# Performance work log

Measured on AMD Instinct MI355X. Metric: run time of the kernel, lower is better.

The kernel has to match this reference:

```python
import jax, jax.numpy as jnp
import numpy as np

C = 256   # channel
NH = 8    # n_heads
NP = 8    # n_points (n_levels = 1)
HD = C // NH


def conv1x1(x, W, b):
    # x: [B,C,H,W], W: [Cout,Cin] -> 1x1 conv == channel-mixing GEMM
    return jnp.einsum('bchw,oc->bohw', x, W) + b[None, :, None, None]


def linear(x, W, b):
    # x: [B,Q,Cin], W: [Cout,Cin] (torch nn.Linear layout)
    return jnp.einsum('bqc,oc->bqo', x, W) + b


def msda(value, loc, attn_w, H, Wd):
    # Multi-scale deformable attention core (single level).
    # value:  [B,Q,NH,HD]  (Q = H*Wd)
    # loc:    [B,Q,NH,NP,2] normalized sampling locations in [0,1] (x,y)
    # attn_w: [B,Q,NH,NP]  softmax weights
    B, Q = value.shape[0], value.shape[1]
    v = jnp.transpose(value, (0, 2, 1, 3))  # [B,NH,HW,HD]
    # grid_sample(align_corners=False): pixel coord = loc*size - 0.5
    ix = loc[..., 0] * Wd - 0.5
    iy = loc[..., 1] * H - 0.5
    x0 = jnp.floor(ix)
    y0 = jnp.floor(iy)

    def gather(xi, yi, wgt):
        valid = ((xi >= 0) & (xi < Wd) & (yi >= 0) & (yi < H)).astype(wgt.dtype)
        xc = jnp.clip(xi, 0, Wd - 1).astype(jnp.int32)
        yc = jnp.clip(yi, 0, H - 1).astype(jnp.int32)
        idx = yc * Wd + xc                                  # [B,Q,NH,NP]
        idx = jnp.transpose(idx, (0, 2, 1, 3)).reshape(B, NH, Q * NP)
        s = jnp.take_along_axis(v, idx[..., None], axis=2)  # [B,NH,Q*NP,HD]
        s = s.reshape(B, NH, Q, NP, HD)
        w = jnp.transpose(wgt * valid, (0, 2, 1, 3))[..., None]
        return s * w

    acc = (gather(x0, y0, (x0 + 1 - ix) * (y0 + 1 - iy))
           + gather(x0 + 1, y0, (ix - x0) * (y0 + 1 - iy))
           + gather(x0, y0 + 1, (x0 + 1 - ix) * (iy - y0))
           + gather(x0 + 1, y0 + 1, (ix - x0) * (iy - y0)))
    aw = jnp.transpose(attn_w, (0, 2, 1, 3))[..., None]      # [B,NH,Q,NP,1]
    out = (acc * aw).sum(axis=3)                             # [B,NH,Q,HD]
    return jnp.transpose(out, (0, 2, 1, 3)).reshape(B, Q, C)


def setup_inputs() -> dict:
    key = jax.random.key(0)
    ks = jax.random.split(key, 24)
    B, H, W = 2, 128, 128

    def w(k, shape, s=0.02):
        return jax.random.normal(k, shape, jnp.float32) * s

    d = {
        'xt': jax.random.normal(ks[0], (B, C, H, W), jnp.float32),
        'xt_1': jax.random.normal(ks[1], (B, C, H, W), jnp.float32),
        'W_in1': w(ks[2], (C, C)), 'b_in1': jnp.zeros((C,), jnp.float32),
        'W_in2': w(ks[3], (C, C)), 'b_in2': jnp.zeros((C,), jnp.float32),
        'Wv': w(ks[4], (C, C)), 'bv': jnp.zeros((C,), jnp.float32),
        'Ws': w(ks[5], (NH * NP * 2, C)), 'bs_off': w(ks[6], (NH * NP * 2,), 1.0),
        'Wa': w(ks[7], (NH * NP, C)), 'ba': jnp.zeros((NH * NP,), jnp.float32),
        'Wo': w(ks[8], (C, C)), 'bo': jnp.zeros((C,), jnp.float32),
        'Wt1': w(ks[9], (C, C)), 'bt1': jnp.zeros((C,), jnp.float32),
        'Wt2': w(ks[10], (C, C)), 'bt2': jnp.zeros((C,), jnp.float32),
        'Wout': w(ks[11], (C, C)), 'bout': jnp.zeros((C,), jnp.float32),
    }
    return d


def reference(xt, xt_1, W_in1, b_in1, W_in2, b_in2, Wv, bv, Ws, bs_off,
              Wa, ba, Wo, bo, Wt1, bt1, Wt2, bt2, Wout, bout):
    x1 = conv1x1(xt, W_in1, b_in1)
    x2 = conv1x1(xt_1, W_in2, b_in2)
    B, _, H, Wd = x1.shape
    Q = H * Wd
    q = jnp.transpose(x1, (0, 2, 3, 1)).reshape(B, Q, C)       # queries
    vflat = jnp.transpose(x2, (0, 2, 3, 1)).reshape(B, Q, C)   # values

    value = linear(vflat, Wv, bv).reshape(B, Q, NH, HD)
    offsets = linear(q, Ws, bs_off).reshape(B, Q, NH, NP, 2)
    attn = jax.nn.softmax(linear(q, Wa, ba).reshape(B, Q, NH, NP), axis=-1)

    # reference points at pixel centers, normalized (x,y)
    gy, gx = jnp.meshgrid(jnp.arange(H), jnp.arange(Wd), indexing='ij')
    ref = jnp.stack([(gx.reshape(-1) + 0.5) / Wd,
                     (gy.reshape(-1) + 0.5) / H], axis=-1).astype(jnp.float32)
    norm = jnp.array([Wd, H], jnp.float32)
    loc = ref[None, :, None, None, :] + offsets / norm          # [B,Q,NH,NP,2]

    out = msda(value, loc, attn, H, Wd)                         # [B,Q,C]
    xt_star = jnp.transpose(linear(out, Wo, bo), (0, 2, 1)).reshape(B, C, H, Wd)

    tg = conv1x1(jax.nn.relu(conv1x1(x1 * xt_star, Wt1, bt1)), Wt2, bt2)
    return jax.nn.relu(conv1x1(x1 + tg, Wout, bout))
```

## Files before the change

kernel.cpp:

```cpp
#include <hip/hip_runtime.h>
#include <math.h>


#define PIX 16384
#define BATCH 2
#define CH 256

typedef short bf16x8 __attribute__((ext_vector_type(8)));
typedef float f32x4 __attribute__((ext_vector_type(4)));

typedef const __attribute__((address_space(1))) void* as1cv;
typedef __attribute__((address_space(3))) void* as3v;
__device__ __forceinline__ void gl_lds16(const void* g, void* l) {
  __builtin_amdgcn_global_load_lds((as1cv)g, (as3v)l, 16, 0, 0);
}

__device__ __forceinline__ ushort f2bf(float f) {
  union { float f; unsigned u; } v; v.f = f;
  unsigned u = v.u;
  unsigned r = u + 0x7fffu + ((u >> 16) & 1u);
  return (ushort)(r >> 16);
}
__device__ __forceinline__ float bfl(unsigned u) {
  union { unsigned u; float f; } v; v.u = u << 16; return v.f;
}
__device__ __forceinline__ float bfh(unsigned u) {
  union { unsigned u; float f; } v; v.u = u & 0xffff0000u; return v.f;
}
__device__ __forceinline__ unsigned fuse_u32(unsigned a, unsigned b, bool mul) {
  float rl = mul ? bfl(a) * bfl(b) : bfl(a) + bfl(b);
  float rh = mul ? bfh(a) * bfh(b) : bfh(a) + bfh(b);
  return (unsigned)f2bf(rl) | ((unsigned)f2bf(rh) << 16);
}

__global__ __launch_bounds__(256) void prep_k(
    const float* __restrict__ xt, const float* __restrict__ xt_1,
    ushort* __restrict__ s0, ushort* __restrict__ s1,
    const float* __restrict__ W_in1, const float* __restrict__ Wo,
    const float* __restrict__ Wt1, const float* __restrict__ Wt2,
    const float* __restrict__ Wout, const float* __restrict__ Ws,
    const float* __restrict__ Wa, const float* __restrict__ bs_off,
    const float* __restrict__ ba, ushort* __restrict__ wb,
    float* __restrict__ bsa,
    const float* __restrict__ Wv, const float* __restrict__ W_in2,
    const float* __restrict__ b_in2, const float* __restrict__ bv,
    ushort* __restrict__ wvp, float* __restrict__ bvp)
{
  __shared__ float lds[32][33];
  const int bid = blockIdx.x;
  const int tid = threadIdx.x;

  if (bid < 16384) {
    const int z = bid >> 12;
    const int rem = bid & 4095;
    const int pblk = rem & 511, cblk = rem >> 9;
    const int b = z & 1;
    const float* in = (z < 2) ? xt : xt_1;
    ushort* out = (z < 2) ? s0 : s1;
    const int p0 = pblk * 32, c0 = cblk * 32;
    const int tx = tid & 31, ty = tid >> 5;
    const float* inb = in + (size_t)b * CH * PIX;
    #pragma unroll
    for (int i = 0; i < 4; ++i)
      lds[ty + i * 8][tx] = inb[(size_t)(c0 + ty + i * 8) * PIX + p0 + tx];
    __syncthreads();
    const int cx = (tid & 15) * 2, py = tid >> 4;
    ushort* outb = out + (size_t)b * PIX * CH;
    #pragma unroll
    for (int i = 0; i < 2; ++i) {
      int pl = py + i * 16;
      unsigned lo = f2bf(lds[cx][pl]);
      unsigned hi = f2bf(lds[cx + 1][pl]);
      *(unsigned*)(outb + (size_t)(p0 + pl) * CH + c0 + cx) = lo | (hi << 16);
    }
  } else if (bid < 16384 + 1473) {
    const int blk = bid - 16384;
    const int k = tid;
    if (blk >= 1472) {
      if (k < 128) bsa[k] = bs_off[k];
      else if (k < 192) bsa[k] = ba[k - 128];
      return;
    }
    const float* src;
    if (blk < 256) src = W_in1 + (size_t)blk * 256;
    else if (blk < 512) src = Wo + (size_t)(blk - 256) * 256;
    else if (blk < 768) src = Wt1 + (size_t)(blk - 512) * 256;
    else if (blk < 1024) src = Wt2 + (size_t)(blk - 768) * 256;
    else if (blk < 1280) src = Wout + (size_t)(blk - 1024) * 256;
    else if (blk < 1408) src = Ws + (size_t)(blk - 1280) * 256;
    else src = Wa + (size_t)(blk - 1408) * 256;
    wb[(size_t)blk * 256 + k] = f2bf(src[k]);
  } else {
    const int o = bid - (16384 + 1473 + 256 - 256) - 1473 - 16384 + 0;
    const int oo = bid - 17857;
    const int k = tid;
    float acc = 0.f;
    #pragma unroll 8
    for (int c = 0; c < 256; ++c)
      acc += Wv[(size_t)oo * 256 + c] * W_in2[(size_t)c * 256 + k];
    wvp[(size_t)oo * 256 + k] = f2bf(acc);
    float* red = &lds[0][0];
    red[k] = Wv[(size_t)oo * 256 + k] * b_in2[k];
    __syncthreads();
    for (int s = 128; s > 0; s >>= 1) {
      if (k < s) red[k] += red[k + s];
      __syncthreads();
    }
    if (k == 0) bvp[oo] = red[0] + bv[oo];
    (void)o;
  }
}

template<int FUSE, bool RELU, int OMODE>
__global__ __launch_bounds__(256, 4) void gemm2_k(
    const ushort* __restrict__ in, const ushort* __restrict__ in2,
    const ushort* __restrict__ Wb, const float* __restrict__ bias,
    void* __restrict__ out, int ldo, size_t obstride)
{
  constexpr int SMEMSZ = (OMODE == 0) ? 24576 : 34816;
  __shared__ __align__(16) char smem[SMEMSZ];
  const int tid = threadIdx.x;
  const int b = blockIdx.z;
  const int p0 = blockIdx.x * 128;
  const int o0 = blockIdx.y * 64;

  const ushort* inb = in + (size_t)b * PIX * CH;

  const int srow = tid >> 2;
  const int sseg = tid & 3;
  const int swz0 = (srow >> 1) & 3;
  const int swz1 = ((srow + 64) >> 1) & 3;
  const int gseg0 = (FUSE == 0) ? (sseg ^ swz0) : sseg;
  const int gseg1 = (FUSE == 0) ? (sseg ^ swz1) : sseg;
  const ushort* xsrc0 = inb + (size_t)(p0 + srow) * CH + gseg0 * 8;
  const ushort* xsrc1 = inb + (size_t)(p0 + srow + 64) * CH + gseg1 * 8;
  const ushort* x2src0 = (FUSE != 0)
      ? in2 + (size_t)b * PIX * CH + (size_t)(p0 + srow) * CH + sseg * 8 : (const ushort*)nullptr;
  const ushort* x2src1 = (FUSE != 0)
      ? in2 + (size_t)b * PIX * CH + (size_t)(p0 + srow + 64) * CH + sseg * 8 : (const ushort*)nullptr;
  const ushort* wsrc = Wb + (size_t)(o0 + srow) * CH + gseg0 * 8;

  const int l = tid & 63, wv = tid >> 6;
  const int lr = l & 15, g4 = l >> 4;

  f32x4 acc[2][4];
  #pragma unroll
  for (int i = 0; i < 2; ++i)
    #pragma unroll
    for (int j = 0; j < 4; ++j) acc[i][j] = (f32x4){0.f, 0.f, 0.f, 0.f};

  uint4 xr[2], x2r[2], wr;

#define STAGE_GLL(buf, kb)                                                     \
  {                                                                            \
    gl_lds16(xsrc0 + (kb), smem + (buf) * 8192 + tid * 16);                    \
    gl_lds16(xsrc1 + (kb), smem + (buf) * 8192 + 4096 + tid * 16);             \
    gl_lds16(wsrc + (kb), smem + 16384 + (buf) * 4096 + tid * 16);             \
  }

#define LOADT(kb)                                                              \
  {                                                                            \
    xr[0] = *(const uint4*)(xsrc0 + (kb));                                     \
    xr[1] = *(const uint4*)(xsrc1 + (kb));                                     \
    x2r[0] = *(const uint4*)(x2src0 + (kb));                                   \
    x2r[1] = *(const uint4*)(x2src1 + (kb));                                   \
    wr = *(const uint4*)(wsrc + (kb));                                         \
  }

#define WRITET(buf)                                                            \
  {                                                                            \
    _Pragma("unroll")                                                          \
    for (int r = 0; r < 2; ++r) {                                              \
      uint4 v = xr[r];                                                         \
      unsigned* pa = (unsigned*)&v;                                            \
      const unsigned* pb = (const unsigned*)&x2r[r];                           \
      _Pragma("unroll")                                                        \
      for (int w = 0; w < 4; ++w) pa[w] = fuse_u32(pa[w], pb[w], FUSE == 1);   \
      const int sw = r ? swz1 : swz0;                                          \
      *(uint4*)(smem + (buf) * 8192 + r * 4096 + srow * 64 +                   \
                ((sseg ^ sw) * 16)) = v;                                       \
    }                                                                          \
    *(uint4*)(smem + 16384 + (buf) * 4096 + srow * 64 +                        \
              ((sseg ^ swz0) * 16)) = wr;                                      \
  }

  if (FUSE == 0) { STAGE_GLL(0, 0) }
  else           { LOADT(0) WRITET(0) }
  __syncthreads();

  for (int t = 0; t < 8; ++t) {
    if (t < 7) {
      if (FUSE == 0) { STAGE_GLL((t + 1) & 1, (t + 1) * 32) }
      else           { LOADT((t + 1) * 32) }
    }
    const char* XB = smem + (t & 1) * 8192;
    const char* WB = smem + 16384 + (t & 1) * 4096;
    bf16x8 af[2], bfr[4];
    #pragma unroll
    for (int fm = 0; fm < 2; ++fm) {
      const int p = wv * 32 + fm * 16 + lr;
      af[fm] = *(const bf16x8*)(XB + p * 64 + ((g4 ^ ((p >> 1) & 3)) * 16));
    }
    #pragma unroll
    for (int fn = 0; fn < 4; ++fn) {
      const int o = fn * 16 + lr;
      bfr[fn] = *(const bf16x8*)(WB + o * 64 + ((g4 ^ ((o >> 1) & 3)) * 16));
    }
    #pragma unroll
    for (int fm = 0; fm < 2; ++fm)
      #pragma unroll
      for (int fn = 0; fn < 4; ++fn)
        acc[fm][fn] = __builtin_amdgcn_mfma_f32_16x16x32_bf16(af[fm], bfr[fn], acc[fm][fn], 0, 0, 0);
    if (t < 7 && FUSE != 0) { WRITET((t + 1) & 1) }
    __syncthreads();
  }
#undef STAGE_GLL
#undef LOADT
#undef WRITET

  float bvv[4];
  #pragma unroll
  for (int fn = 0; fn < 4; ++fn) bvv[fn] = bias[o0 + fn * 16 + lr];

  if (OMODE == 1) {
    float* El2 = (float*)smem;
    #pragma unroll
    for (int fm = 0; fm < 2; ++fm)
      #pragma unroll
      for (int fn = 0; fn < 4; ++fn) {
        float4 v;
        v.x = acc[fm][fn][0] + bvv[fn]; v.y = acc[fm][fn][1] + bvv[fn];
        v.z = acc[fm][fn][2] + bvv[fn]; v.w = acc[fm][fn][3] + bvv[fn];
        if (RELU) {
          v.x = fmaxf(v.x, 0.f); v.y = fmaxf(v.y, 0.f);
          v.z = fmaxf(v.z, 0.f); v.w = fmaxf(v.w, 0.f);
        }
        *(float4*)&El2[(size_t)(fn * 16 + lr) * 132 + wv * 32 + fm * 16 + g4 * 4] = v;
      }
    __syncthreads();
    float* outb = (float*)out + (size_t)b * obstride;
    const int og = tid >> 5, seg = tid & 31;
    #pragma unroll
    for (int r = 0; r < 8; ++r) {
      const int orow = og + r * 8;
      float4 v = *(float4*)(smem + orow * 528 + seg * 16);
      *(float4*)(outb + (size_t)(o0 + orow) * ldo + p0 + seg * 4) = v;
    }
  } else {
    ushort* El = (ushort*)smem;
    #pragma unroll
    for (int fm = 0; fm < 2; ++fm)
      #pragma unroll
      for (int fn = 0; fn < 4; ++fn)
        #pragma unroll
        for (int r = 0; r < 4; ++r) {
          const int p = wv * 32 + fm * 16 + g4 * 4 + r;
          float v = acc[fm][fn][r] + bvv[fn];
          if (RELU) v = fmaxf(v, 0.f);
          El[p * 72 + fn * 16 + lr] = f2bf(v);
        }
    __syncthreads();
    ushort* outb = (ushort*)out + (size_t)b * obstride;
    const int rg = tid >> 3, seg = tid & 7;
    #pragma unroll
    for (int r = 0; r < 4; ++r) {
      const int row = rg + r * 32;
      uint4 v = *(uint4*)(smem + row * 144 + seg * 16);
      *(uint4*)(outb + (size_t)(p0 + row) * ldo + o0 + seg * 8) = v;
    }
  }
}

__global__ __launch_bounds__(256, 4) void gemm2_dual_k(
    const ushort* __restrict__ inA, const ushort* __restrict__ inB,
    const ushort* __restrict__ WbA, const ushort* __restrict__ WbB,
    const float* __restrict__ biasA, const float* __restrict__ biasB,
    ushort* __restrict__ outA, ushort* __restrict__ outB)
{
  __shared__ __align__(16) char smem[24576];
  const int tid = threadIdx.x;
  const int b = blockIdx.z;
  const int p0 = blockIdx.x * 128;
  const bool second = blockIdx.y >= 4;
  const int o0 = (blockIdx.y & 3) * 64;
  const ushort* in = second ? inB : inA;
  const ushort* Wb = second ? WbB : WbA;
  const float* bias = second ? biasB : biasA;
  ushort* out = second ? outB : outA;

  const ushort* inb = in + (size_t)b * PIX * CH;

  const int srow = tid >> 2;
  const int sseg = tid & 3;
  const int swz0 = (srow >> 1) & 3;
  const int swz1 = ((srow + 64) >> 1) & 3;
  const int gseg0 = sseg ^ swz0;
  const int gseg1 = sseg ^ swz1;
  const ushort* xsrc0 = inb + (size_t)(p0 + srow) * CH + gseg0 * 8;
  const ushort* xsrc1 = inb + (size_t)(p0 + srow + 64) * CH + gseg1 * 8;
  const ushort* wsrc = Wb + (size_t)(o0 + srow) * CH + gseg0 * 8;

  const int l = tid & 63, wv = tid >> 6;
  const int lr = l & 15, g4 = l >> 4;

  f32x4 acc[2][4];
  #pragma unroll
  for (int i = 0; i < 2; ++i)
    #pragma unroll
    for (int j = 0; j < 4; ++j) acc[i][j] = (f32x4){0.f, 0.f, 0.f, 0.f};

#define STAGE_GLL(buf, kb)                                                     \
  {                                                                            \
    gl_lds16(xsrc0 + (kb), smem + (buf) * 8192 + tid * 16);                    \
    gl_lds16(xsrc1 + (kb), smem + (buf) * 8192 + 4096 + tid * 16);             \
    gl_lds16(wsrc + (kb), smem + 16384 + (buf) * 4096 + tid * 16);             \
  }

  STAGE_GLL(0, 0)
  __syncthreads();

  for (int t = 0; t < 8; ++t) {
    if (t < 7) { STAGE_GLL((t + 1) & 1, (t + 1) * 32) }
    const char* XB = smem + (t & 1) * 8192;
    const char* WB = smem + 16384 + (t & 1) * 4096;
    bf16x8 af[2], bfr[4];
    #pragma unroll
    for (int fm = 0; fm < 2; ++fm) {
      const int p = wv * 32 + fm * 16 + lr;
      af[fm] = *(const bf16x8*)(XB + p * 64 + ((g4 ^ ((p >> 1) & 3)) * 16));
    }
    #pragma unroll
    for (int fn = 0; fn < 4; ++fn) {
      const int o = fn * 16 + lr;
      bfr[fn] = *(const bf16x8*)(WB + o * 64 + ((g4 ^ ((o >> 1) & 3)) * 16));
    }
    #pragma unroll
    for (int fm = 0; fm < 2; ++fm)
      #pragma unroll
      for (int fn = 0; fn < 4; ++fn)
        acc[fm][fn] = __builtin_amdgcn_mfma_f32_16x16x32_bf16(af[fm], bfr[fn], acc[fm][fn], 0, 0, 0);
    __syncthreads();
  }
#undef STAGE_GLL

  float bvv[4];
  #pragma unroll
  for (int fn = 0; fn < 4; ++fn) bvv[fn] = bias[o0 + fn * 16 + lr];

  ushort* El = (ushort*)smem;
  #pragma unroll
  for (int fm = 0; fm < 2; ++fm)
    #pragma unroll
    for (int fn = 0; fn < 4; ++fn)
      #pragma unroll
      for (int r = 0; r < 4; ++r) {
        const int p = wv * 32 + fm * 16 + g4 * 4 + r;
        El[p * 72 + fn * 16 + lr] = f2bf(acc[fm][fn][r] + bvv[fn]);
      }
  __syncthreads();
  ushort* outb = out + (size_t)b * PIX * CH;
  const int rg = tid >> 3, seg = tid & 7;
  #pragma unroll
  for (int r = 0; r < 4; ++r) {
    const int row = rg + r * 32;
    uint4 v = *(uint4*)(smem + row * 144 + seg * 16);
    *(uint4*)(outb + (size_t)(p0 + row) * CH + o0 + seg * 8) = v;
  }
}

__global__ __launch_bounds__(256) void msda_k(
    const ushort* __restrict__ value, const ushort* __restrict__ sa,
    ushort* __restrict__ out)
{
  const int t = blockIdx.x * 256 + threadIdx.x;
  const int dh = t & 1;
  const int h = (t >> 1) & 7;
  const int pg = t >> 4;
  const int b = pg >> 14;
  const int p = pg & (PIX - 1);
  const int px = p & 127, py = p >> 7;

  const ushort* vb = value + (size_t)b * PIX * CH;
  const ushort* sp = sa + (size_t)pg * 192;

  uint4 lgv = *(const uint4*)(sp + 128 + h * 8);
  const unsigned* lgw = (const unsigned*)&lgv;
  float lg[8];
  #pragma unroll
  for (int i = 0; i < 4; ++i) { lg[2 * i] = bfl(lgw[i]); lg[2 * i + 1] = bfh(lgw[i]); }
  float m = lg[0];
  #pragma unroll
  for (int i = 1; i < 8; ++i) m = fmaxf(m, lg[i]);
  float s = 0.f;
  #pragma unroll
  for (int i = 0; i < 8; ++i) { lg[i] = __expf(lg[i] - m); s += lg[i]; }
  const float inv = 1.f / s;

  uint4 ov0 = *(const uint4*)(sp + h * 16);
  uint4 ov1 = *(const uint4*)(sp + h * 16 + 8);
  float of[16];
  {
    const unsigned* ow = (const unsigned*)&ov0;
    #pragma unroll
    for (int i = 0; i < 4; ++i) { of[2 * i] = bfl(ow[i]); of[2 * i + 1] = bfh(ow[i]); }
    const unsigned* ow1 = (const unsigned*)&ov1;
    #pragma unroll
    for (int i = 0; i < 4; ++i) { of[8 + 2 * i] = bfl(ow1[i]); of[8 + 2 * i + 1] = bfh(ow1[i]); }
  }

  float acc[16];
  #pragma unroll
  for (int i = 0; i < 16; ++i) acc[i] = 0.f;

  #pragma unroll
  for (int pt = 0; pt < 8; ++pt) {
    const float ox = of[2 * pt], oy = of[2 * pt + 1];
    const float aw = lg[pt] * inv;
    const float ix = px + ox, iy = py + oy;
    const float xf = floorf(ix), yf = floorf(iy);
    const float fx = ix - xf, fy = iy - yf;
    const int x0 = (int)xf, y0 = (int)yf;
    #pragma unroll
    for (int cr = 0; cr < 4; ++cr) {
      const int dx = cr & 1, dy = cr >> 1;
      const int xx = x0 + dx, yy = y0 + dy;
      const float wx = dx ? fx : (1.f - fx);
      const float wy = dy ? fy : (1.f - fy);
      const bool valid = ((unsigned)xx < 128u) & ((unsigned)yy < 128u);
      float w = valid ? (wx * wy * aw) : 0.f;
      const int xc = min(max(xx, 0), 127), yc = min(max(yy, 0), 127);
      const ushort* vr = vb + ((size_t)(yc * 128 + xc) * CH + h * 32 + dh * 16);
      uint4 q0 = *(const uint4*)vr;
      uint4 q1 = *(const uint4*)(vr + 8);
      const unsigned* qw0 = (const unsigned*)&q0;
      const unsigned* qw1 = (const unsigned*)&q1;
      #pragma unroll
      for (int ww = 0; ww < 4; ++ww) {
        acc[2 * ww + 0] = fmaf(w, bfl(qw0[ww]), acc[2 * ww + 0]);
        acc[2 * ww + 1] = fmaf(w, bfh(qw0[ww]), acc[2 * ww + 1]);
        acc[8 + 2 * ww + 0] = fmaf(w, bfl(qw1[ww]), acc[8 + 2 * ww + 0]);
        acc[8 + 2 * ww + 1] = fmaf(w, bfh(qw1[ww]), acc[8 + 2 * ww + 1]);
      }
    }
  }
  unsigned r[8];
  #pragma unroll
  for (int k = 0; k < 8; ++k)
    r[k] = (unsigned)f2bf(acc[2 * k]) | ((unsigned)f2bf(acc[2 * k + 1]) << 16);
  ushort* dst = out + (size_t)pg * CH + h * 32 + dh * 16;
  *(uint4*)dst = *(uint4*)&r[0];
  *(uint4*)(dst + 8) = *(uint4*)&r[4];
}

extern "C" void kernel_launch(void* const* d_in, const int* in_sizes, int n_in,
                              void* d_out, int out_size, void* d_ws, size_t ws_size,
                              hipStream_t stream)
{
  const float* xt     = (const float*)d_in[0];
  const float* xt_1   = (const float*)d_in[1];
  const float* W_in1  = (const float*)d_in[2];
  const float* b_in1  = (const float*)d_in[3];
  const float* W_in2  = (const float*)d_in[4];
  const float* b_in2  = (const float*)d_in[5];
  const float* Wv     = (const float*)d_in[6];
  const float* bv     = (const float*)d_in[7];
  const float* Ws     = (const float*)d_in[8];
  const float* bs_off = (const float*)d_in[9];
  const float* Wa     = (const float*)d_in[10];
  const float* ba     = (const float*)d_in[11];
  const float* Wo     = (const float*)d_in[12];
  const float* bo     = (const float*)d_in[13];
  const float* Wt1    = (const float*)d_in[14];
  const float* bt1    = (const float*)d_in[15];
  const float* Wt2    = (const float*)d_in[16];
  const float* bt2    = (const float*)d_in[17];
  const float* Wout   = (const float*)d_in[18];
  const float* bout   = (const float*)d_in[19];

  char* ws = (char*)d_ws;
  const size_t SLOT = (size_t)BATCH * PIX * CH * 2;
  const size_t SAB  = (size_t)BATCH * PIX * 192 * 2;
  ushort* s0 = (ushort*)(ws + 0 * SLOT);
  ushort* s1 = (ushort*)(ws + 1 * SLOT);
  ushort* s2 = (ushort*)(ws + 2 * SLOT);
  ushort* s3 = (ushort*)(ws + 3 * SLOT);
  ushort* s4 = (ushort*)(ws + 4 * SLOT);
  ushort* sa = (ushort*)(ws + 5 * SLOT);
  char* wbase = ws + 5 * SLOT + SAB;
  ushort* wb  = (ushort*)wbase;
  ushort* wvp = (ushort*)(wbase + (size_t)1472 * 256 * 2);
  float* bsa  = (float*)(wbase + (size_t)1472 * 256 * 2 + (size_t)256 * 256 * 2);
  float* bvp  = bsa + 192;

  ushort* wb_in1 = wb;
  ushort* wb_o   = wb + 65536;
  ushort* wb_t1  = wb + 131072;
  ushort* wb_t2  = wb + 196608;
  ushort* wb_out = wb + 262144;
  ushort* wb_sa  = wb + 327680;

  dim3 blk(256);
  dim3 gD(PIX / 128, 8, BATCH);
  dim3 gF(PIX / 128, 4, BATCH);
  dim3 gS(PIX / 128, 3, BATCH);
  const size_t OBS = (size_t)PIX * CH;

  prep_k<<<18113, blk, 0, stream>>>(xt, xt_1, s0, s1,
      W_in1, Wo, Wt1, Wt2, Wout, Ws, Wa, bs_off, ba, wb, bsa,
      Wv, W_in2, b_in2, bv, wvp, bvp);

  gemm2_dual_k<<<gD, blk, 0, stream>>>(s0, s1, wb_in1, wvp, b_in1, bvp, s2, s3);
  gemm2_k<0, false, 0><<<gS, blk, 0, stream>>>(s2, nullptr, wb_sa, bsa, sa, 192, (size_t)PIX * 192);
  msda_k<<<dim3((BATCH * PIX * 16) / 256), blk, 0, stream>>>(s3, sa, s4);
  gemm2_k<0, false, 0><<<gF, blk, 0, stream>>>(s4, nullptr, wb_o, bo, s0, CH, OBS);
  gemm2_k<1, true , 0><<<gF, blk, 0, stream>>>(s0, s2, wb_t1, bt1, s1, CH, OBS);
  gemm2_k<0, false, 0><<<gF, blk, 0, stream>>>(s1, nullptr, wb_t2, bt2, s3, CH, OBS);
  gemm2_k<2, true , 1><<<gF, blk, 0, stream>>>(s3, s2, wb_out, bout, d_out, PIX, (size_t)CH * PIX);
}
```

Measured before the change: 155.2 us.

## Fuse back-to-back GEMM pairs into one kernel keeping intermediates in LDS

Replaces four separate 1x1-conv GEMM launches (Wo, Wt1, Wt2, Wout) with two fused kernels. Each kernel loads a 32-pixel tile of input and x1 into LDS, computes the first GEMM, writes its bf16 result back into LDS, then applies the elementwise fuse with x1 and the second GEMM. This removes two full intermediate round trips to global memory and two launches. In exchange each block uses 64KB of LDS, which lowers occupancy, and the tiles are smaller with weights re-streamed per block. The gemm2_k paths for FUSE and OMODE 1 are deleted as no longer used.

```diff
diff --git a/kernel.cpp b/kernel.cpp
--- a/kernel.cpp
+++ b/kernel.cpp
@@ -91,7 +91,6 @@
     else src = Wa + (size_t)(blk - 1408) * 256;
     wb[(size_t)blk * 256 + k] = f2bf(src[k]);
   } else {
-    const int o = bid - (16384 + 1473 + 256 - 256) - 1473 - 16384 + 0;
     const int oo = bid - 17857;
     const int k = tid;
     float acc = 0.f;
@@ -107,7 +106,6 @@
       __syncthreads();
     }
     if (k == 0) bvp[oo] = red[0] + bv[oo];
-    (void)o;
   }
 }
 
@@ -117,8 +115,7 @@
     const ushort* __restrict__ Wb, const float* __restrict__ bias,
     void* __restrict__ out, int ldo, size_t obstride)
 {
-  constexpr int SMEMSZ = (OMODE == 0) ? 24576 : 34816;
-  __shared__ __align__(16) char smem[SMEMSZ];
+  __shared__ __align__(16) char smem[24576];
   const int tid = threadIdx.x;
   const int b = blockIdx.z;
   const int p0 = blockIdx.x * 128;
@@ -130,14 +127,10 @@
   const int sseg = tid & 3;
   const int swz0 = (srow >> 1) & 3;
   const int swz1 = ((srow + 64) >> 1) & 3;
-  const int gseg0 = (FUSE == 0) ? (sseg ^ swz0) : sseg;
-  const int gseg1 = (FUSE == 0) ? (sseg ^ swz1) : sseg;
+  const int gseg0 = sseg ^ swz0;
+  const int gseg1 = sseg ^ swz1;
   const ushort* xsrc0 = inb + (size_t)(p0 + srow) * CH + gseg0 * 8;
   const ushort* xsrc1 = inb + (size_t)(p0 + srow + 64) * CH + gseg1 * 8;
-  const ushort* x2src0 = (FUSE != 0)
-      ? in2 + (size_t)b * PIX * CH + (size_t)(p0 + srow) * CH + sseg * 8 : (const ushort*)nullptr;
-  const ushort* x2src1 = (FUSE != 0)
-      ? in2 + (size_t)b * PIX * CH + (size_t)(p0 + srow + 64) * CH + sseg * 8 : (const ushort*)nullptr;
   const ushort* wsrc = Wb + (size_t)(o0 + srow) * CH + gseg0 * 8;
 
   const int l = tid & 63, wv = tid >> 6;
@@ -148,8 +141,6 @@
   for (int i = 0; i < 2; ++i)
     #pragma unroll
     for (int j = 0; j < 4; ++j) acc[i][j] = (f32x4){0.f, 0.f, 0.f, 0.f};
-
-  uint4 xr[2], x2r[2], wr;
 
 #define STAGE_GLL(buf, kb)                                                     \
   {                                                                            \
@@ -158,41 +149,11 @@
     gl_lds16(wsrc + (kb), smem + 16384 + (buf) * 4096 + tid * 16);             \
   }
 
-#define LOADT(kb)                                                              \
-  {                                                                            \
-    xr[0] = *(const uint4*)(xsrc0 + (kb));                                     \
-    xr[1] = *(const uint4*)(xsrc1 + (kb));                                     \
-    x2r[0] = *(const uint4*)(x2src0 + (kb));                                   \
-    x2r[1] = *(const uint4*)(x2src1 + (kb));                                   \
-    wr = *(const uint4*)(wsrc + (kb));                                         \
-  }
-
-#define WRITET(buf)                                                            \
-  {                                                                            \
-    _Pragma("unroll")                                                          \
-    for (int r = 0; r < 2; ++r) {                                              \
-      uint4 v = xr[r];                                                         \
-      unsigned* pa = (unsigned*)&v;                                            \
-      const unsigned* pb = (const unsigned*)&x2r[r];                           \
-      _Pragma("unroll")                                                        \
-      for (int w = 0; w < 4; ++w) pa[w] = fuse_u32(pa[w], pb[w], FUSE == 1);   \
-      const int sw = r ? swz1 : swz0;                                          \
-      *(uint4*)(smem + (buf) * 8192 + r * 4096 + srow * 64 +                   \
-                ((sseg ^ sw) * 16)) = v;                                       \
-    }                                                                          \
-    *(uint4*)(smem + 16384 + (buf) * 4096 + srow * 64 +                        \
-              ((sseg ^ swz0) * 16)) = wr;                                      \
-  }
-
-  if (FUSE == 0) { STAGE_GLL(0, 0) }
-  else           { LOADT(0) WRITET(0) }
+  STAGE_GLL(0, 0)
   __syncthreads();
 
   for (int t = 0; t < 8; ++t) {
-    if (t < 7) {
-      if (FUSE == 0) { STAGE_GLL((t + 1) & 1, (t + 1) * 32) }
-      else           { LOADT((t + 1) * 32) }
-    }
+    if (t < 7) { STAGE_GLL((t + 1) & 1, (t + 1) * 32) }
     const char* XB = smem + (t & 1) * 8192;
     const char* WB = smem + 16384 + (t & 1) * 4096;
     bf16x8 af[2], bfr[4];
@@ -211,63 +172,34 @@
       #pragma unroll
       for (int fn = 0; fn < 4; ++fn)
         acc[fm][fn] = __builtin_amdgcn_mfma_f32_16x16x32_bf16(af[fm], bfr[fn], acc[fm][fn], 0, 0, 0);
-    if (t < 7 && FUSE != 0) { WRITET((t + 1) & 1) }
     __syncthreads();
   }
 #undef STAGE_GLL
-#undef LOADT
-#undef WRITET
 
   float bvv[4];
   #pragma unroll
   for (int fn = 0; fn < 4; ++fn) bvv[fn] = bias[o0 + fn * 16 + lr];
 
-  if (OMODE == 1) {
-    float* El2 = (float*)smem;
-    #pragma unroll
-    for (int fm = 0; fm < 2; ++fm)
-      #pragma unroll
-      for (int fn = 0; fn < 4; ++fn) {
-        float4 v;
-        v.x = acc[fm][fn][0] + bvv[fn]; v.y = acc[fm][fn][1] + bvv[fn];
-        v.z = acc[fm][fn][2] + bvv[fn]; v.w = acc[fm][fn][3] + bvv[fn];
-        if (RELU) {
-          v.x = fmaxf(v.x, 0.f); v.y = fmaxf(v.y, 0.f);
-          v.z = fmaxf(v.z, 0.f); v.w = fmaxf(v.w, 0.f);
-        }
-        *(float4*)&El2[(size_t)(fn * 16 + lr) * 132 + wv * 32 + fm * 16 + g4 * 4] = v;
+  ushort* El = (ushort*)smem;
+  #pragma unroll
+  for (int fm = 0; fm < 2; ++fm)
+    #pragma unroll
+    for (int fn = 0; fn < 4; ++fn)
+      #pragma unroll
+      for (int r = 0; r < 4; ++r) {
+        const int p = wv * 32 + fm * 16 + g4 * 4 + r;
+        float v = acc[fm][fn][r] + bvv[fn];
+        if (RELU) v = fmaxf(v, 0.f);
+        El[p * 72 + fn * 16 + lr] = f2bf(v);
       }
-    __syncthreads();
-    float* outb = (float*)out + (size_t)b * obstride;
-    const int og = tid >> 5, seg = tid & 31;
-    #pragma unroll
-    for (int r = 0; r < 8; ++r) {
-      const int orow = og + r * 8;
-      float4 v = *(float4*)(smem + orow * 528 + seg * 16);
-      *(float4*)(outb + (size_t)(o0 + orow) * ldo + p0 + seg * 4) = v;
-    }
-  } else {
-    ushort* El = (ushort*)smem;
-    #pragma unroll
-    for (int fm = 0; fm < 2; ++fm)
-      #pragma unroll
-      for (int fn = 0; fn < 4; ++fn)
-        #pragma unroll
-        for (int r = 0; r < 4; ++r) {
-          const int p = wv * 32 + fm * 16 + g4 * 4 + r;
-          float v = acc[fm][fn][r] + bvv[fn];
-          if (RELU) v = fmaxf(v, 0.f);
-          El[p * 72 + fn * 16 + lr] = f2bf(v);
-        }
-    __syncthreads();
-    ushort* outb = (ushort*)out + (size_t)b * obstride;
-    const int rg = tid >> 3, seg = tid & 7;
-    #pragma unroll
-    for (int r = 0; r < 4; ++r) {
-      const int row = rg + r * 32;
-      uint4 v = *(uint4*)(smem + row * 144 + seg * 16);
-      *(uint4*)(outb + (size_t)(p0 + row) * ldo + o0 + seg * 8) = v;
-    }
+  __syncthreads();
+  ushort* outb = (ushort*)out + (size_t)b * obstride;
+  const int rg = tid >> 3, seg = tid & 7;
+  #pragma unroll
+  for (int r = 0; r < 4; ++r) {
+    const int row = rg + r * 32;
+    uint4 v = *(uint4*)(smem + row * 144 + seg * 16);
+    *(uint4*)(outb + (size_t)(p0 + row) * ldo + o0 + seg * 8) = v;
   }
 }
 
@@ -366,6 +298,141 @@
     uint4 v = *(uint4*)(smem + row * 144 + seg * 16);
     *(uint4*)(outb + (size_t)(p0 + row) * CH + o0 + seg * 8) = v;
   }
+}
+
+template<int F2, bool RELU2, int OM2>
+__global__ __launch_bounds__(256, 2) void fused2_k(
+    const ushort* __restrict__ IN, const ushort* __restrict__ X1,
+    const ushort* __restrict__ W1b, const float* __restrict__ b1,
+    const ushort* __restrict__ W2b, const float* __restrict__ b2,
+    void* __restrict__ OUT)
+{
+  __shared__ __align__(16) char smem[65536];
+  const int tid = threadIdx.x;
+  const int b = blockIdx.z;
+  const int p0 = blockIdx.x * 32;
+
+  const ushort* inb = IN + (size_t)b * PIX * CH;
+  const ushort* x1b = X1 + (size_t)b * PIX * CH;
+
+  const int trow = tid >> 5, tcc = tid & 31;
+  const int wrA = tid >> 2, wcc = tid & 3;
+  const int wkey = (tid >> 3) & 3;
+  const int wgc = wcc ^ wkey;
+
+  const int l = tid & 63, w = tid >> 6;
+  const int pm = w & 1, oh = w >> 1;
+  const int lr = l & 15, g4 = l >> 4;
+
+#define STAGE_W2(Wsrc, buf, oc, t)                                             \
+  {                                                                            \
+    gl_lds16(Wsrc + (size_t)((oc) * 128 + wrA) * CH + (t) * 32 + wgc * 8,      \
+             smem + 49152 + (buf) * 8192 + tid * 16);                          \
+    gl_lds16(Wsrc + (size_t)((oc) * 128 + 64 + wrA) * CH + (t) * 32 + wgc * 8, \
+             smem + 49152 + (buf) * 8192 + 4096 + tid * 16);                   \
+  }
+
+  #pragma unroll
+  for (int j = 0; j < 4; ++j) {
+    const int r = j * 8 + trow;
+    gl_lds16(inb + (size_t)(p0 + r) * CH + ((tcc ^ (r & 7)) * 8),
+             smem + j * 4096 + tid * 16);
+    gl_lds16(x1b + (size_t)(p0 + r) * CH + ((tcc ^ (r & 7)) * 8),
+             smem + 16384 + j * 4096 + tid * 16);
+  }
+
+  f32x4 acc[4];
+
+  for (int stage = 0; stage < 2; ++stage) {
+    const ushort* Wsrc = stage ? W2b : W1b;
+    const float* bb = stage ? b2 : b1;
+    for (int oc = 0; oc < 2; ++oc) {
+      STAGE_W2(Wsrc, 0, oc, 0)
+      __syncthreads();
+      #pragma unroll
+      for (int i = 0; i < 4; ++i) acc[i] = (f32x4){0.f, 0.f, 0.f, 0.f};
+      float bv[4];
+      #pragma unroll
+      for (int fn = 0; fn < 4; ++fn) bv[fn] = bb[oc * 128 + oh * 64 + fn * 16 + lr];
+
+      for (int t = 0; t < 8; ++t) {
+        if (t < 7) STAGE_W2(Wsrc, (t + 1) & 1, oc, t + 1)
+        const char* WB = smem + 49152 + (t & 1) * 8192;
+        const int p = pm * 16 + lr, c = t * 4 + g4;
+        const int fro = ((c ^ (p & 7)) * 16);
+        bf16x8 af;
+        if (stage == 0) {
+          af = *(const bf16x8*)(smem + p * 512 + fro);
+        } else {
+          bf16x8 a1 = *(const bf16x8*)(smem + 16384 + p * 512 + fro);
+          bf16x8 aT = *(const bf16x8*)(smem + 32768 + p * 512 + fro);
+          unsigned rr[4];
+          const unsigned* u1 = (const unsigned*)&a1;
+          const unsigned* uT = (const unsigned*)&aT;
+          #pragma unroll
+          for (int q = 0; q < 4; ++q) rr[q] = fuse_u32(u1[q], uT[q], F2 == 1);
+          af = *(bf16x8*)&rr[0];
+        }
+        bf16x8 bfr[4];
+        #pragma unroll
+        for (int fn = 0; fn < 4; ++fn) {
+          const int o = oh * 64 + fn * 16 + lr;
+          bfr[fn] = *(const bf16x8*)(WB + o * 64 + ((g4 ^ ((o >> 1) & 3)) * 16));
+        }
+        #pragma unroll
+        for (int fn = 0; fn < 4; ++fn)
+          acc[fn] = __builtin_amdgcn_mfma_f32_16x16x32_bf16(af, bfr[fn], acc[fn], 0, 0, 0);
+        __syncthreads();
+      }
+
+      if (stage == 0) {
+        #pragma unroll
+        for (int fn = 0; fn < 4; ++fn)
+          #pragma unroll
+          for (int r = 0; r < 4; ++r) {
+            const int p = pm * 16 + g4 * 4 + r;
+            const int o = oc * 128 + oh * 64 + fn * 16 + lr;
+            *(ushort*)(smem + 32768 + p * 512 + (((o >> 3) ^ (p & 7)) * 16) + (o & 7) * 2)
+                = f2bf(acc[fn][r] + bv[fn]);
+          }
+      } else if (OM2 == 1) {
+        float* outb = (float*)OUT + (size_t)b * CH * PIX;
+        #pragma unroll
+        for (int fn = 0; fn < 4; ++fn) {
+          float4 v;
+          v.x = acc[fn][0] + bv[fn]; v.y = acc[fn][1] + bv[fn];
+          v.z = acc[fn][2] + bv[fn]; v.w = acc[fn][3] + bv[fn];
+          if (RELU2) {
+            v.x = fmaxf(v.x, 0.f); v.y = fmaxf(v.y, 0.f);
+            v.z = fmaxf(v.z, 0.f); v.w = fmaxf(v.w, 0.f);
+          }
+          *(float4*)(outb + (size_t)(oc * 128 + oh * 64 + fn * 16 + lr) * PIX
+                     + p0 + pm * 16 + g4 * 4) = v;
+        }
+      } else {
+        __syncthreads();
+        ushort* El = (ushort*)smem;
+        #pragma unroll
+        for (int fn = 0; fn < 4; ++fn)
+          #pragma unroll
+          for (int r = 0; r < 4; ++r) {
+            const int p = pm * 16 + g4 * 4 + r;
+            const int o = oh * 64 + fn * 16 + lr;
+            float v = acc[fn][r] + bv[fn];
+            if (RELU2) v = fmaxf(v, 0.f);
+            El[p * 136 + o] = f2bf(v);
+          }
+        __syncthreads();
+        ushort* outb = (ushort*)OUT + (size_t)b * PIX * CH;
+        const int row = tid >> 3, seg = tid & 7;
+        uint4 v0 = *(uint4*)(smem + row * 272 + seg * 32);
+        uint4 v1 = *(uint4*)(smem + row * 272 + seg * 32 + 16);
+        *(uint4*)(outb + (size_t)(p0 + row) * CH + oc * 128 + seg * 16) = v0;
+        *(uint4*)(outb + (size_t)(p0 + row) * CH + oc * 128 + seg * 16 + 8) = v1;
+      }
+    }
+  }
+#undef STAGE_W2
 }
 
 __global__ __launch_bounds__(256) void msda_k(
@@ -501,9 +568,8 @@
 
   dim3 blk(256);
   dim3 gD(PIX / 128, 8, BATCH);
-  dim3 gF(PIX / 128, 4, BATCH);
   dim3 gS(PIX / 128, 3, BATCH);
-  const size_t OBS = (size_t)PIX * CH;
+  dim3 gFu(PIX / 32, 1, BATCH);
 
   prep_k<<<18113, blk, 0, stream>>>(xt, xt_1, s0, s1,
       W_in1, Wo, Wt1, Wt2, Wout, Ws, Wa, bs_off, ba, wb, bsa,
@@ -512,8 +578,6 @@
   gemm2_dual_k<<<gD, blk, 0, stream>>>(s0, s1, wb_in1, wvp, b_in1, bvp, s2, s3);
   gemm2_k<0, false, 0><<<gS, blk, 0, stream>>>(s2, nullptr, wb_sa, bsa, sa, 192, (size_t)PIX * 192);
   msda_k<<<dim3((BATCH * PIX * 16) / 256), blk, 0, stream>>>(s3, sa, s4);
-  gemm2_k<0, false, 0><<<gF, blk, 0, stream>>>(s4, nullptr, wb_o, bo, s0, CH, OBS);
-  gemm2_k<1, true , 0><<<gF, blk, 0, stream>>>(s0, s2, wb_t1, bt1, s1, CH, OBS);
-  gemm2_k<0, false, 0><<<gF, blk, 0, stream>>>(s1, nullptr, wb_t2, bt2, s3, CH, OBS);
-  gemm2_k<2, true , 1><<<gF, blk, 0, stream>>>(s3, s2, wb_out, bout, d_out, PIX, (size_t)CH * PIX);
-}
+  fused2_k<1, true, 0><<<gFu, blk, 0, stream>>>(s4, s2, wb_o, bo, wb_t1, bt1, s1);
+  fused2_k<2, true, 1><<<gFu, blk, 0, stream>>>(s1, s2, wb_t2, bt2, wb_out, bout, d_out);
+}
```

Result: slower. 171.3 us (+10.4%).

## Load GEMM MFMA operands directly from global memory instead of LDS staging

Applied to the files above, without the earlier changes.

Removes the double-buffered LDS staging (global_load_lds and the swizzled register-to-LDS writes) from all bf16 GEMM kernels. Each lane now reads its MFMA A and B fragments straight from global memory with 16-byte loads, and the K loop is fully unrolled with no barriers. Launch-bounds occupancy hints are dropped and the shared memory is shrunk to the epilogue size. This avoids LDS traffic and synchronisation, but each weight fragment is now re-read from global or cache by every wave, and loads are less coalesced (16 B per row per lane).

```diff
diff --git a/kernel.cpp b/kernel.cpp
--- a/kernel.cpp
+++ b/kernel.cpp
@@ -8,12 +8,6 @@
 
 typedef short bf16x8 __attribute__((ext_vector_type(8)));
 typedef float f32x4 __attribute__((ext_vector_type(4)));
-
-typedef const __attribute__((address_space(1))) void* as1cv;
-typedef __attribute__((address_space(3))) void* as3v;
-__device__ __forceinline__ void gl_lds16(const void* g, void* l) {
-  __builtin_amdgcn_global_load_lds((as1cv)g, (as3v)l, 16, 0, 0);
-}
 
 __device__ __forceinline__ ushort f2bf(float f) {
   union { float f; unsigned u; } v; v.f = f;
@@ -91,7 +85,6 @@
     else src = Wa + (size_t)(blk - 1408) * 256;
     wb[(size_t)blk * 256 + k] = f2bf(src[k]);
   } else {
-    const int o = bid - (16384 + 1473 + 256 - 256) - 1473 - 16384 + 0;
     const int oo = bid - 17857;
     const int k = tid;
     float acc = 0.f;
@@ -107,116 +100,64 @@
       __syncthreads();
     }
     if (k == 0) bvp[oo] = red[0] + bv[oo];
-    (void)o;
   }
 }
 
 template<int FUSE, bool RELU, int OMODE>
-__global__ __launch_bounds__(256, 4) void gemm2_k(
+__global__ __launch_bounds__(256) void gemm3_k(
     const ushort* __restrict__ in, const ushort* __restrict__ in2,
     const ushort* __restrict__ Wb, const float* __restrict__ bias,
     void* __restrict__ out, int ldo, size_t obstride)
 {
-  constexpr int SMEMSZ = (OMODE == 0) ? 24576 : 34816;
+  constexpr int SMEMSZ = (OMODE == 0) ? 18432 : 34816;
   __shared__ __align__(16) char smem[SMEMSZ];
   const int tid = threadIdx.x;
   const int b = blockIdx.z;
   const int p0 = blockIdx.x * 128;
   const int o0 = blockIdx.y * 64;
 
-  const ushort* inb = in + (size_t)b * PIX * CH;
-
-  const int srow = tid >> 2;
-  const int sseg = tid & 3;
-  const int swz0 = (srow >> 1) & 3;
-  const int swz1 = ((srow + 64) >> 1) & 3;
-  const int gseg0 = (FUSE == 0) ? (sseg ^ swz0) : sseg;
-  const int gseg1 = (FUSE == 0) ? (sseg ^ swz1) : sseg;
-  const ushort* xsrc0 = inb + (size_t)(p0 + srow) * CH + gseg0 * 8;
-  const ushort* xsrc1 = inb + (size_t)(p0 + srow + 64) * CH + gseg1 * 8;
-  const ushort* x2src0 = (FUSE != 0)
-      ? in2 + (size_t)b * PIX * CH + (size_t)(p0 + srow) * CH + sseg * 8 : (const ushort*)nullptr;
-  const ushort* x2src1 = (FUSE != 0)
-      ? in2 + (size_t)b * PIX * CH + (size_t)(p0 + srow + 64) * CH + sseg * 8 : (const ushort*)nullptr;
-  const ushort* wsrc = Wb + (size_t)(o0 + srow) * CH + gseg0 * 8;
-
   const int l = tid & 63, wv = tid >> 6;
   const int lr = l & 15, g4 = l >> 4;
 
+  const ushort* arow = in + (size_t)b * PIX * CH + (size_t)(p0 + wv * 32 + lr) * CH + g4 * 8;
+  const ushort* a2row = (FUSE != 0)
+      ? in2 + (size_t)b * PIX * CH + (size_t)(p0 + wv * 32 + lr) * CH + g4 * 8
+      : (const ushort*)nullptr;
+  const ushort* wrow = Wb + (size_t)(o0 + lr) * CH + g4 * 8;
+
   f32x4 acc[2][4];
   #pragma unroll
   for (int i = 0; i < 2; ++i)
     #pragma unroll
     for (int j = 0; j < 4; ++j) acc[i][j] = (f32x4){0.f, 0.f, 0.f, 0.f};
 
-  uint4 xr[2], x2r[2], wr;
-
-#define STAGE_GLL(buf, kb)                                                     \
-  {                                                                            \
-    gl_lds16(xsrc0 + (kb), smem + (buf) * 8192 + tid * 16);                    \
-    gl_lds16(xsrc1 + (kb), smem + (buf) * 8192 + 4096 + tid * 16);             \
-    gl_lds16(wsrc + (kb), smem + 16384 + (buf) * 4096 + tid * 16);             \
-  }
-
-#define LOADT(kb)                                                              \
-  {                                                                            \
-    xr[0] = *(const uint4*)(xsrc0 + (kb));                                     \
-    xr[1] = *(const uint4*)(xsrc1 + (kb));                                     \
-    x2r[0] = *(const uint4*)(x2src0 + (kb));                                   \
-    x2r[1] = *(const uint4*)(x2src1 + (kb));                                   \
-    wr = *(const uint4*)(wsrc + (kb));                                         \
-  }
-
-#define WRITET(buf)                                                            \
-  {                                                                            \
-    _Pragma("unroll")                                                          \
-    for (int r = 0; r < 2; ++r) {                                              \
-      uint4 v = xr[r];                                                         \
-      unsigned* pa = (unsigned*)&v;                                            \
-      const unsigned* pb = (const unsigned*)&x2r[r];                           \
-      _Pragma("unroll")                                                        \
-      for (int w = 0; w < 4; ++w) pa[w] = fuse_u32(pa[w], pb[w], FUSE == 1);   \
-      const int sw = r ? swz1 : swz0;                                          \
-      *(uint4*)(smem + (buf) * 8192 + r * 4096 + srow * 64 +                   \
-                ((sseg ^ sw) * 16)) = v;                                       \
-    }                                                                          \
-    *(uint4*)(smem + 16384 + (buf) * 4096 + srow * 64 +                        \
-              ((sseg ^ swz0) * 16)) = wr;                                      \
-  }
-
-  if (FUSE == 0) { STAGE_GLL(0, 0) }
-  else           { LOADT(0) WRITET(0) }
-  __syncthreads();
-
+  #pragma unroll
   for (int t = 0; t < 8; ++t) {
-    if (t < 7) {
-      if (FUSE == 0) { STAGE_GLL((t + 1) & 1, (t + 1) * 32) }
-      else           { LOADT((t + 1) * 32) }
-    }
-    const char* XB = smem + (t & 1) * 8192;
-    const char* WB = smem + 16384 + (t & 1) * 4096;
     bf16x8 af[2], bfr[4];
     #pragma unroll
     for (int fm = 0; fm < 2; ++fm) {
-      const int p = wv * 32 + fm * 16 + lr;
-      af[fm] = *(const bf16x8*)(XB + p * 64 + ((g4 ^ ((p >> 1) & 3)) * 16));
-    }
-    #pragma unroll
-    for (int fn = 0; fn < 4; ++fn) {
-      const int o = fn * 16 + lr;
-      bfr[fn] = *(const bf16x8*)(WB + o * 64 + ((g4 ^ ((o >> 1) & 3)) * 16));
-    }
+      bf16x8 a = *(const bf16x8*)(arow + (size_t)fm * 16 * CH + t * 32);
+      if (FUSE != 0) {
+        bf16x8 a2 = *(const bf16x8*)(a2row + (size_t)fm * 16 * CH + t * 32);
+        unsigned rr[4];
+        const unsigned* u1 = (const unsigned*)&a;
+        const unsigned* u2 = (const unsigned*)&a2;
+        #pragma unroll
+        for (int q = 0; q < 4; ++q) rr[q] = fuse_u32(u1[q], u2[q], FUSE == 1);
+        af[fm] = *(bf16x8*)&rr[0];
+      } else {
+        af[fm] = a;
+      }
+    }
+    #pragma unroll
+    for (int fn = 0; fn < 4; ++fn)
+      bfr[fn] = *(const bf16x8*)(wrow + (size_t)fn * 16 * CH + t * 32);
     #pragma unroll
     for (int fm = 0; fm < 2; ++fm)
       #pragma unroll
       for (int fn = 0; fn < 4; ++fn)
         acc[fm][fn] = __builtin_amdgcn_mfma_f32_16x16x32_bf16(af[fm], bfr[fn], acc[fm][fn], 0, 0, 0);
-    if (t < 7 && FUSE != 0) { WRITET((t + 1) & 1) }
-    __syncthreads();
-  }
-#undef STAGE_GLL
-#undef LOADT
-#undef WRITET
+  }
 
   float bvv[4];
   #pragma unroll
@@ -271,13 +212,13 @@
   }
 }
 
-__global__ __launch_bounds__(256, 4) void gemm2_dual_k(
+__global__ __launch_bounds__(256) void gemm3_dual_k(
     const ushort* __restrict__ inA, const ushort* __restrict__ inB,
     const ushort* __restrict__ WbA, const ushort* __restrict__ WbB,
     const float* __restrict__ biasA, const float* __restrict__ biasB,
     ushort* __restrict__ outA, ushort* __restrict__ outB)
 {
-  __shared__ __align__(16) char smem[24576];
+  __shared__ __align__(16) char smem[18432];
   const int tid = threadIdx.x;
   const int b = blockIdx.z;
   const int p0 = blockIdx.x * 128;
@@ -288,60 +229,33 @@
   const float* bias = second ? biasB : biasA;
   ushort* out = second ? outB : outA;
 
-  const ushort* inb = in + (size_t)b * PIX * CH;
-
-  const int srow = tid >> 2;
-  const int sseg = tid & 3;
-  const int swz0 = (srow >> 1) & 3;
-  const int swz1 = ((srow + 64) >> 1) & 3;
-  const int gseg0 = sseg ^ swz0;
-  const int gseg1 = sseg ^ swz1;
-  const ushort* xsrc0 = inb + (size_t)(p0 + srow) * CH + gseg0 * 8;
-  const ushort* xsrc1 = inb + (size_t)(p0 + srow + 64) * CH + gseg1 * 8;
-  const ushort* wsrc = Wb + (size_t)(o0 + srow) * CH + gseg0 * 8;
-
   const int l = tid & 63, wv = tid >> 6;
   const int lr = l & 15, g4 = l >> 4;
 
+  const ushort* arow = in + (size_t)b * PIX * CH + (size_t)(p0 + wv * 32 + lr) * CH + g4 * 8;
+  const ushort* wrow = Wb + (size_t)(o0 + lr) * CH + g4 * 8;
+
   f32x4 acc[2][4];
   #pragma unroll
   for (int i = 0; i < 2; ++i)
     #pragma unroll
     for (int j = 0; j < 4; ++j) acc[i][j] = (f32x4){0.f, 0.f, 0.f, 0.f};
 
-#define STAGE_GLL(buf, kb)                                                     \
-  {                                                                            \
-    gl_lds16(xsrc0 + (kb), smem + (buf) * 8192 + tid * 16);                    \
-    gl_lds16(xsrc1 + (kb), smem + (buf) * 8192 + 4096 + tid * 16);             \
-    gl_lds16(wsrc + (kb), smem + 16384 + (buf) * 4096 + tid * 16);             \
-  }
-
-  STAGE_GLL(0, 0)
-  __syncthreads();
-
+  #pragma unroll
   for (int t = 0; t < 8; ++t) {
-    if (t < 7) { STAGE_GLL((t + 1) & 1, (t + 1) * 32) }
-    const char* XB = smem + (t & 1) * 8192;
-    const char* WB = smem + 16384 + (t & 1) * 4096;
     bf16x8 af[2], bfr[4];
     #pragma unroll
-    for (int fm = 0; fm < 2; ++fm) {
-      const int p = wv * 32 + fm * 16 + lr;
-      af[fm] = *(const bf16x8*)(XB + p * 64 + ((g4 ^ ((p >> 1) & 3)) * 16));
-    }
-    #pragma unroll
-    for (int fn = 0; fn < 4; ++fn) {
-      const int o = fn * 16 + lr;
-      bfr[fn] = *(const bf16x8*)(WB + o * 64 + ((g4 ^ ((o >> 1) & 3)) * 16));
-    }
+    for (int fm = 0; fm < 2; ++fm)
+      af[fm] = *(const bf16x8*)(arow + (size_t)fm * 16 * CH + t * 32);
+    #pragma unroll
+    for (int fn = 0; fn < 4; ++fn)
+      bfr[fn] = *(const bf16x8*)(wrow + (size_t)fn * 16 * CH + t * 32);
     #pragma unroll
     for (int fm = 0; fm < 2; ++fm)
       #pragma unroll
       for (int fn = 0; fn < 4; ++fn)
         acc[fm][fn] = __builtin_amdgcn_mfma_f32_16x16x32_bf16(af[fm], bfr[fn], acc[fm][fn], 0, 0, 0);
-    __syncthreads();
-  }
-#undef STAGE_GLL
+  }
 
   float bvv[4];
   #pragma unroll
@@ -509,11 +423,11 @@
       W_in1, Wo, Wt1, Wt2, Wout, Ws, Wa, bs_off, ba, wb, bsa,
       Wv, W_in2, b_in2, bv, wvp, bvp);
 
-  gemm2_dual_k<<<gD, blk, 0, stream>>>(s0, s1, wb_in1, wvp, b_in1, bvp, s2, s3);
-  gemm2_k<0, false, 0><<<gS, blk, 0, stream>>>(s2, nullptr, wb_sa, bsa, sa, 192, (size_t)PIX * 192);
+  gemm3_dual_k<<<gD, blk, 0, stream>>>(s0, s1, wb_in1, wvp, b_in1, bvp, s2, s3);
+  gemm3_k<0, false, 0><<<gS, blk, 0, stream>>>(s2, nullptr, wb_sa, bsa, sa, 192, (size_t)PIX * 192);
   msda_k<<<dim3((BATCH * PIX * 16) / 256), blk, 0, stream>>>(s3, sa, s4);
-  gemm2_k<0, false, 0><<<gF, blk, 0, stream>>>(s4, nullptr, wb_o, bo, s0, CH, OBS);
-  gemm2_k<1, true , 0><<<gF, blk, 0, stream>>>(s0, s2, wb_t1, bt1, s1, CH, OBS);
-  gemm2_k<0, false, 0><<<gF, blk, 0, stream>>>(s1, nullptr, wb_t2, bt2, s3, CH, OBS);
-  gemm2_k<2, true , 1><<<gF, blk, 0, stream>>>(s3, s2, wb_out, bout, d_out, PIX, (size_t)CH * PIX);
-}
+  gemm3_k<0, false, 0><<<gF, blk, 0, stream>>>(s4, nullptr, wb_o, bo, s0, CH, OBS);
+  gemm3_k<1, true , 0><<<gF, blk, 0, stream>>>(s0, s2, wb_t1, bt1, s1, CH, OBS);
+  gemm3_k<0, false, 0><<<gF, blk, 0, stream>>>(s1, nullptr, wb_t2, bt2, s3, CH, OBS);
+  gemm3_k<2, true , 1><<<gF, blk, 0, stream>>>(s3, s2, wb_out, bout, d_out, PIX, (size_t)CH * PIX);
+}
```

New measurement: 254.2 us. 1.64x slower.
